# Kernel optimization log

Measured on AMD Instinct MI355X. Metric: run time of the kernel, lower is better.

Reference implementation:

```python
import jax, jax.numpy as jnp
import numpy as np

B, T, D = 4, 2048, 2048
H, G, HD = 16, 4, 128
NB, BS = 512, 16  # num_blocks, block_size
GS = H // G
SCALE = HD ** -0.5
NEG = -1e30


def setup_inputs() -> dict:
    key = jax.random.key(0)
    ks = jax.random.split(key, 5)
    x = jax.random.normal(ks[0], (B, T, D), dtype=jnp.float32)
    block_tables = jnp.arange(B * (T // BS), dtype=jnp.int32).reshape(B, T // BS)
    kv_lens = jnp.zeros((B,), dtype=jnp.int32)
    k_blocks = jnp.zeros((NB, G, BS, HD), jnp.float32)
    v_blocks = jnp.zeros((NB, G, BS, HD), jnp.float32)
    w_q = jax.random.normal(ks[1], (D, H * HD), jnp.float32) * 0.02
    w_k = jax.random.normal(ks[2], (D, G * HD), jnp.float32) * 0.02
    w_v = jax.random.normal(ks[3], (D, G * HD), jnp.float32) * 0.02
    w_o = jax.random.normal(ks[4], (H * HD, D), jnp.float32) * 0.02
    return {"x": x, "w_q": w_q, "w_k": w_k, "w_v": w_v, "w_o": w_o,
            "k_blocks": k_blocks, "v_blocks": v_blocks,
            "block_tables": block_tables, "kv_lens": kv_lens}


def reference(x, w_q, w_k, w_v, w_o, k_blocks, v_blocks, block_tables, kv_lens):
    # projections
    q = (x @ w_q).reshape(B, T, H, HD).transpose(0, 2, 1, 3)   # [B,H,T,Hd]
    k = (x @ w_k).reshape(B, T, G, HD).transpose(0, 2, 1, 3)   # [B,G,T,Hd]
    v = (x @ w_v).reshape(B, T, G, HD).transpose(0, 2, 1, 3)

    # paged cache append (vectorized scatter over [B,T])
    pos = kv_lens[:, None] + jnp.arange(T)                     # [B,T]
    slot, off = pos // BS, pos % BS
    bid = jnp.take_along_axis(block_tables, slot, axis=1)      # [B,T] block ids
    k_blocks = k_blocks.at[bid, :, off, :].set(k.transpose(0, 2, 1, 3))
    v_blocks = v_blocks.at[bid, :, off, :].set(v.transpose(0, 2, 1, 3))

    # gather contiguous KV per request; prefill: kv_lens == 0 -> seq_len = T
    S = T
    nb = (S + BS - 1) // BS
    blk = block_tables[:, :nb]                                 # [B,nb]
    k_seq = k_blocks[blk].transpose(0, 2, 1, 3, 4).reshape(B, G, nb * BS, HD)[:, :, :S]
    v_seq = v_blocks[blk].transpose(0, 2, 1, 3, 4).reshape(B, G, nb * BS, HD)[:, :, :S]

    # original's flat reshapes pair head h with kv group (h % G)
    qg = q.reshape(B, GS, G, T, HD)
    scores = jnp.einsum('bjgqd,bgkd->bjgqk', qg, k_seq) * SCALE

    q_pos = (S - T) + jnp.arange(T)
    k_pos = jnp.arange(S)
    causal = k_pos[None, :] <= q_pos[:, None]                  # [T,S]
    scores = jnp.where(causal, scores, NEG)
    attn = jax.nn.softmax(scores, axis=-1)

    out = jnp.einsum('bjgqk,bgkd->bjgqd', attn, v_seq)         # [B,GS,G,T,Hd]
    out = out.reshape(B, H, T, HD).transpose(0, 2, 1, 3).reshape(B, T, H * HD)
    return out @ w_o
```

## Files before the change

### kernel.cpp

```cpp
#include <hip/hip_runtime.h>
#include <stdint.h>

typedef __attribute__((ext_vector_type(8))) short short8;
typedef __attribute__((ext_vector_type(8))) unsigned short ushort8;
typedef __attribute__((ext_vector_type(4))) float f32x4;

__device__ __forceinline__ ushort f2bf(float f) {
  union { float f; uint32_t u; } v; v.f = f;
  uint32_t r = v.u + 0x7FFFu + ((v.u >> 16) & 1u);
  return (ushort)(r >> 16);
}

__device__ __forceinline__ ushort f2bf_trunc(float f) {
  union { float f; uint32_t u; } v; v.f = f;
  return (ushort)(v.u >> 16);
}

__device__ __forceinline__ float fexp2(float x) {
  float r;
  asm("v_exp_f32 %0, %1" : "=v"(r) : "v"(x));
  return r;
}

__device__ __forceinline__ void gld16(const ushort* g, ushort* l) {
  __builtin_amdgcn_global_load_lds((const __attribute__((address_space(1))) void*)g,
                                   (__attribute__((address_space(3))) void*)l, 16, 0, 0);
}

__global__ __launch_bounds__(256) void k_f32_to_bf16(const float* __restrict__ in,
                                                     ushort* __restrict__ out, long n) {
  long i = ((long)blockIdx.x * 256 + threadIdx.x) * 8;
  if (i >= n) return;
  float4 a = *(const float4*)(in + i);
  float4 b = *(const float4*)(in + i + 4);
  ushort8 o;
  o[0] = f2bf(a.x); o[1] = f2bf(a.y); o[2] = f2bf(a.z); o[3] = f2bf(a.w);
  o[4] = f2bf(b.x); o[5] = f2bf(b.y); o[6] = f2bf(b.z); o[7] = f2bf(b.w);
  *(ushort8*)(out + i) = o;
}

__global__ __launch_bounds__(256) void k_w_transpose(const float* __restrict__ in,
                                                     ushort* __restrict__ out, int R, int C) {
  __shared__ float t[32][33];
  int tx = threadIdx.x & 31, ty = threadIdx.x >> 5;
  int r0 = blockIdx.y * 32, c0 = blockIdx.x * 32;
#pragma unroll
  for (int i = 0; i < 4; i++)
    t[ty + i * 8][tx] = in[(size_t)(r0 + ty + i * 8) * C + c0 + tx];
  __syncthreads();
#pragma unroll
  for (int i = 0; i < 4; i++)
    out[(size_t)(c0 + ty + i * 8) * R + r0 + tx] = f2bf(t[tx][ty + i * 8]);
}

__global__ __launch_bounds__(256) void k_v_transpose(const ushort* __restrict__ qkv,
                                                     ushort* __restrict__ out) {
  __shared__ ushort t[32][33];
  int tx = threadIdx.x & 31, ty = threadIdx.x >> 5;
  int t0 = blockIdx.x * 32, d0 = blockIdx.y * 32;
  int b = blockIdx.z >> 2, g = blockIdx.z & 3;
#pragma unroll
  for (int i = 0; i < 4; i++)
    t[ty + i * 8][tx] =
        qkv[((size_t)b * 2048 + t0 + ty + i * 8) * 3072 + 2560 + g * 128 + d0 + tx];
  __syncthreads();
#pragma unroll
  for (int i = 0; i < 4; i++)
    out[(((size_t)b * 4 + g) * 128 + d0 + ty + i * 8) * 2048 + t0 + tx] = t[tx][ty + i * 8];
}

__device__ __forceinline__ void stage256(const ushort* G, int ldg, ushort* Ls, int tid) {
  int l = tid & 63, w = tid >> 6;
  int rsub = l >> 3;
  int cs = ((l & 7) ^ rsub) << 3;
#pragma unroll
  for (int n = 0; n < 4; n++) {
    int c = n * 8 + w;
    gld16(G + (size_t)(c * 8 + rsub) * ldg + cs, Ls + c * 512 + l * 8);
  }
}

template <int F32OUT>
__global__ __launch_bounds__(512) void k_gemm256(const ushort* __restrict__ A,
                                                 const ushort* __restrict__ BT,
                                                 void* __restrict__ C, int M, int N, int K) {
  __shared__ ushort As0[256 * 64], As1[256 * 64];
  __shared__ ushort Bs0[256 * 64], Bs1[256 * 64];
  const int tid = threadIdx.x;
  const int lane = tid & 63, wid = tid >> 6;
  const int wm = wid >> 2, wn = wid & 3;
  const int l15 = lane & 15, l4 = lane >> 4;
  const int rsw = (l15 & 7) << 3;
  int nwg = gridDim.x * gridDim.y;
  int lin = blockIdx.y * gridDim.x + blockIdx.x;
  int swz = (lin & 7) * (nwg >> 3) + (lin >> 3);
  int bx = swz % gridDim.x, by = swz / gridDim.x;
  const int m0 = by * 256, n0 = bx * 256;

  const ushort* Atile = A + (size_t)m0 * K;
  const ushort* Btile = BT + (size_t)n0 * K;
  const int NK = K >> 6;

  f32x4 acc[8][4] = {};

  stage256(Atile, K, As0, tid);
  stage256(Btile, K, Bs0, tid);
  stage256(Atile + 64, K, As1, tid);
  stage256(Btile + 64, K, Bs1, tid);
  asm volatile("s_waitcnt vmcnt(8)" ::: "memory");
  asm volatile("s_barrier" ::: "memory");

  for (int kt = 0; kt < NK; ++kt) {
    const ushort* Ab = (kt & 1) ? As1 : As0;
    const ushort* Bb = (kt & 1) ? Bs1 : Bs0;
    short8 bfrag[4][2];
#pragma unroll
    for (int nf = 0; nf < 4; nf++)
#pragma unroll
      for (int ks = 0; ks < 2; ks++)
        bfrag[nf][ks] = *(const short8*)&Bb[(wn * 64 + nf * 16 + l15) * 64 +
                                            ((ks * 32 + l4 * 8) ^ rsw)];
#pragma unroll
    for (int q = 0; q < 4; q++) {
      short8 afr[2][2];
#pragma unroll
      for (int dm = 0; dm < 2; dm++)
#pragma unroll
        for (int ks = 0; ks < 2; ks++)
          afr[dm][ks] = *(const short8*)&Ab[(wm * 128 + (q * 2 + dm) * 16 + l15) * 64 +
                                            ((ks * 32 + l4 * 8) ^ rsw)];
      __builtin_amdgcn_s_setprio(1);
#pragma unroll
      for (int dm = 0; dm < 2; dm++)
#pragma unroll
        for (int nf = 0; nf < 4; nf++)
#pragma unroll
          for (int ks = 0; ks < 2; ks++)
            acc[q * 2 + dm][nf] = __builtin_amdgcn_mfma_f32_16x16x32_bf16(
                afr[dm][ks], bfrag[nf][ks], acc[q * 2 + dm][nf], 0, 0, 0);
      __builtin_amdgcn_s_setprio(0);
    }
    asm volatile("s_barrier" ::: "memory");
    if (kt + 2 < NK) {
      stage256(Atile + (kt + 2) * 64, K, (kt & 1) ? As1 : As0, tid);
      stage256(Btile + (kt + 2) * 64, K, (kt & 1) ? Bs1 : Bs0, tid);
      asm volatile("s_waitcnt vmcnt(8)" ::: "memory");
    } else {
      asm volatile("s_waitcnt vmcnt(0)" ::: "memory");
    }
    asm volatile("s_barrier" ::: "memory");
  }

#pragma unroll
  for (int mf = 0; mf < 8; mf++)
#pragma unroll
    for (int nf = 0; nf < 4; nf++)
#pragma unroll
      for (int r = 0; r < 4; r++) {
        int m = m0 + wm * 128 + mf * 16 + l4 * 4 + r;
        int n = n0 + wn * 64 + nf * 16 + l15;
        if (F32OUT)
          ((float*)C)[(size_t)m * N + n] = acc[mf][nf][r];
        else
          ((ushort*)C)[(size_t)m * N + n] = f2bf(acc[mf][nf][r]);
      }
}

__device__ __forceinline__ void stage_k8(const ushort* Kt, ushort* Ks, int tid) {
  int l = tid & 63, w = tid >> 6;
#pragma unroll
  for (int n = 0; n < 2; n++) {
    int cidx = w * 2 + n;
    int r = cidx * 4 + (l >> 4);
    int cs = ((l & 15) * 8) ^ ((r & 7) << 3);
    gld16(Kt + (size_t)r * 3072 + cs, Ks + cidx * 512 + l * 8);
  }
}

__device__ __forceinline__ void stage_v8(const ushort* Vt, ushort* Vs, int tid) {
  int l = tid & 63, w = tid >> 6;
#pragma unroll
  for (int n = 0; n < 2; n++) {
    int cidx = w * 2 + n;
    int d = cidx * 8 + (l >> 3);
    int cs = ((l & 7) * 8) ^ ((d & 7) << 3);
    gld16(Vt + (size_t)d * 2048 + cs, Vs + cidx * 512 + l * 8);
  }
}

__global__ __launch_bounds__(512) void k_attn(const ushort* __restrict__ QKV,
                                              const ushort* __restrict__ VT,
                                              ushort* __restrict__ O) {
  const int T = 2048, HD = 128, G = 4, H = 16, RS = 3072;
  const float SCALE2 = 0.08838834764831845f * 1.4426950408889634f;
  int bid = blockIdx.x;
  int pr = bid >> 6;
  int bh = bid & 63;
  int h = bh & 15, b = bh >> 4;
  int g = h & 3;
  int tid = threadIdx.x, wid = tid >> 6, lane = tid & 63;
  int l15 = lane & 15, l4 = lane >> 4;
  int kswz = (l15 & 7) << 3;

  __shared__ __align__(16) char smem[102400];
  ushort* Ks0 = (ushort*)smem;
  ushort* Ks1 = (ushort*)(smem + 16384);
  ushort* Vs0 = (ushort*)(smem + 32768);
  ushort* Vs1 = (ushort*)(smem + 49152);
  ushort* Pw  = (ushort*)(smem + 65536) + wid * (32 * 72);

  const ushort* Qb = &QKV[(size_t)b * T * RS + h * HD];
  const ushort* Kb = &QKV[(size_t)b * T * RS + 2048 + g * HD];
  const ushort* Vb = &VT[((size_t)b * G + g) * (size_t)HD * T];

#pragma unroll 1
  for (int half = 0; half < 2; half++) {
    int ch = half ? pr : (7 - pr);
    int qw = ch * 256 + wid * 32;
    int nt = 4 * (ch + 1);

    short8 qf[2][4];
#pragma unroll
    for (int mf = 0; mf < 2; mf++)
#pragma unroll
      for (int kf = 0; kf < 4; kf++)
        qf[mf][kf] = *(const short8*)&Qb[(size_t)(qw + mf * 16 + l15) * RS + kf * 32 + l4 * 8];

    f32x4 o[2][8] = {};
    float mrow[8], lrow[8];
#pragma unroll
    for (int i = 0; i < 8; i++) { mrow[i] = -3e38f; lrow[i] = 0.f; }

    stage_k8(Kb, Ks0, tid);
    stage_v8(Vb, Vs0, tid);
    __syncthreads();

#pragma unroll 1
    for (int it = 0; it < nt; ++it) {
      int t0 = it * 64;
      int cur = it & 1;
      ushort* Kc = cur ? Ks1 : Ks0;
      ushort* Vc = cur ? Vs1 : Vs0;
      if (it + 1 < nt) {
        stage_k8(Kb + (size_t)(t0 + 64) * RS, cur ? Ks0 : Ks1, tid);
        stage_v8(Vb + t0 + 64, cur ? Vs0 : Vs1, tid);
      }
      if (t0 <= qw + 31) {
        f32x4 s[2][4] = {};
#pragma unroll
        for (int kf = 0; kf < 4; kf++) {
#pragma unroll
          for (int nf = 0; nf < 4; nf++) {
            short8 bk = *(const short8*)&Kc[(nf * 16 + l15) * 128 + ((kf * 32 + l4 * 8) ^ kswz)];
            s[0][nf] = __builtin_amdgcn_mfma_f32_16x16x32_bf16(qf[0][kf], bk, s[0][nf], 0, 0, 0);
            s[1][nf] = __builtin_amdgcn_mfma_f32_16x16x32_bf16(qf[1][kf], bk, s[1][nf], 0, 0, 0);
          }
        }
        bool needmask = (t0 + 63 > qw);
        if (needmask) {
#pragma unroll
          for (int mf = 0; mf < 2; mf++)
#pragma unroll
            for (int nf = 0; nf < 4; nf++)
#pragma unroll
              for (int r = 0; r < 4; r++) {
                int qq = qw + mf * 16 + l4 * 4 + r;
                int kk = t0 + nf * 16 + l15;
                if (kk > qq) s[mf][nf][r] = -1e30f;
              }
        }
        float xs8[8];
        bool ok = true;
#pragma unroll
        for (int mf = 0; mf < 2; mf++)
#pragma unroll
          for (int r = 0; r < 4; r++) {
            int i = mf * 4 + r;
            float x = fmaxf(fmaxf(s[mf][0][r], s[mf][1][r]), fmaxf(s[mf][2][r], s[mf][3][r]));
            x = fmaxf(x, __shfl_xor(x, 1));
            x = fmaxf(x, __shfl_xor(x, 2));
            x = fmaxf(x, __shfl_xor(x, 4));
            x = fmaxf(x, __shfl_xor(x, 8));
            float xs = x * SCALE2;
            xs8[i] = xs;
            ok = ok && (xs <= mrow[i] + 11.5f);
          }
        if (!__all(ok)) {
#pragma unroll
          for (int i = 0; i < 8; i++) {
            float mn = fmaxf(mrow[i], xs8[i]);
            float sc = fexp2(mrow[i] - mn);
            mrow[i] = mn;
            lrow[i] *= sc;
#pragma unroll
            for (int nfo = 0; nfo < 8; nfo++)
              o[i >> 2][nfo][i & 3] *= sc;
          }
        }
        float rs[8];
#pragma unroll
        for (int i = 0; i < 8; i++) rs[i] = 0.f;
#pragma unroll
        for (int mf = 0; mf < 2; mf++)
#pragma unroll
          for (int nf = 0; nf < 4; nf++)
#pragma unroll
            for (int r = 0; r < 4; r++) {
              float pq = fexp2(__builtin_fmaf(s[mf][nf][r], SCALE2, -mrow[mf * 4 + r]));
              rs[mf * 4 + r] += pq;
              Pw[(mf * 16 + l4 * 4 + r) * 72 + nf * 16 + l15] = f2bf_trunc(pq);
            }
#pragma unroll
        for (int i = 0; i < 8; i++) lrow[i] += rs[i];
#pragma unroll
        for (int kf = 0; kf < 2; kf++) {
          short8 pa0 = *(const short8*)&Pw[(l15) * 72 + kf * 32 + l4 * 8];
          short8 pa1 = *(const short8*)&Pw[(16 + l15) * 72 + kf * 32 + l4 * 8];
#pragma unroll
          for (int nfo = 0; nfo < 8; nfo++) {
            short8 bv = *(const short8*)&Vc[(nfo * 16 + l15) * 64 + ((kf * 32 + l4 * 8) ^ kswz)];
            o[0][nfo] = __builtin_amdgcn_mfma_f32_16x16x32_bf16(pa0, bv, o[0][nfo], 0, 0, 0);
            o[1][nfo] = __builtin_amdgcn_mfma_f32_16x16x32_bf16(pa1, bv, o[1][nfo], 0, 0, 0);
          }
        }
      }
      __syncthreads();
    }

#pragma unroll
    for (int i = 0; i < 8; i++) {
      float x = lrow[i];
      x += __shfl_xor(x, 1);
      x += __shfl_xor(x, 2);
      x += __shfl_xor(x, 4);
      x += __shfl_xor(x, 8);
      lrow[i] = x;
    }
    float inv[8];
#pragma unroll
    for (int i = 0; i < 8; i++) inv[i] = 1.0f / lrow[i];
#pragma unroll
    for (int mf = 0; mf < 2; mf++)
#pragma unroll
      for (int nfo = 0; nfo < 8; nfo++)
#pragma unroll
        for (int r = 0; r < 4; r++) {
          int t = qw + mf * 16 + l4 * 4 + r;
          int d = nfo * 16 + l15;
          O[(((size_t)b * T + t) * H + h) * HD + d] = f2bf(o[mf][nfo][r] * inv[mf * 4 + r]);
        }
    __syncthreads();
  }
}

extern "C" void kernel_launch(void* const* d_in, const int* in_sizes, int n_in,
                              void* d_out, int out_size, void* d_ws, size_t ws_size,
                              hipStream_t stream) {
  const float* x   = (const float*)d_in[0];
  const float* w_q = (const float*)d_in[1];
  const float* w_k = (const float*)d_in[2];
  const float* w_v = (const float*)d_in[3];
  const float* w_o = (const float*)d_in[4];

  char* ws = (char*)d_ws;
  ushort* xbf  = (ushort*)(ws);
  ushort* wkvT = (ushort*)(ws + 33554432ul);
  ushort* woT  = (ushort*)(ws + 46137344ul);
  ushort* qkvb = (ushort*)(ws + 54525952ul);
  ushort* VTb  = (ushort*)(ws + 104857600ul);
  ushort* attn = xbf;

  k_f32_to_bf16<<<8192, 256, 0, stream>>>(x, xbf, 16777216L);
  k_w_transpose<<<dim3(64, 64), 256, 0, stream>>>(w_q, wkvT, 2048, 2048);
  k_w_transpose<<<dim3(16, 64), 256, 0, stream>>>(w_k, wkvT + 2048ul * 2048, 2048, 512);
  k_w_transpose<<<dim3(16, 64), 256, 0, stream>>>(w_v, wkvT + 2560ul * 2048, 2048, 512);
  k_w_transpose<<<dim3(64, 64), 256, 0, stream>>>(w_o, woT, 2048, 2048);

  k_gemm256<0><<<dim3(12, 32), 512, 0, stream>>>(xbf, wkvT, qkvb, 8192, 3072, 2048);

  k_v_transpose<<<dim3(64, 4, 16), 256, 0, stream>>>(qkvb, VTb);

  k_attn<<<256, 512, 0, stream>>>(qkvb, VTb, attn);

  k_gemm256<1><<<dim3(8, 32), 512, 0, stream>>>(attn, woT, (float*)d_out, 8192, 2048, 2048);
}
```

Measured before the change: 358.8 us.

## Restructure GEMM into 4-stage K=32 pipeline with interleaved prefetch

Replaces the double-buffered K=64 GEMM with a four-slot ring of K=32 tiles, prefetching three tiles ahead. Loads are split so the B and A prefetches are issued between the two MFMA halves of each step. The LDS layout changes to a fragment-native ordering with no XOR swizzle, and the vmcnt waits are tuned for the tail. It aims to hide global-load latency better and cut barrier stalls, at the cost of more loop iterations, more barriers per unit of K, and possible LDS bank conflicts from the unswizzled layout.

```diff
diff --git a/kernel.cpp b/kernel.cpp
--- a/kernel.cpp
+++ b/kernel.cpp
@@ -69,85 +69,81 @@
     out[(((size_t)b * 4 + g) * 128 + d0 + ty + i * 8) * 2048 + t0 + tx] = t[tx][ty + i * 8];
 }
 
-__device__ __forceinline__ void stage256(const ushort* G, int ldg, ushort* Ls, int tid) {
-  int l = tid & 63, w = tid >> 6;
-  int rsub = l >> 3;
-  int cs = ((l & 7) ^ rsub) << 3;
-#pragma unroll
-  for (int n = 0; n < 4; n++) {
-    int c = n * 8 + w;
-    gld16(G + (size_t)(c * 8 + rsub) * ldg + cs, Ls + c * 512 + l * 8);
-  }
-}
-
 template <int F32OUT>
-__global__ __launch_bounds__(512) void k_gemm256(const ushort* __restrict__ A,
-                                                 const ushort* __restrict__ BT,
-                                                 void* __restrict__ C, int M, int N, int K) {
-  __shared__ ushort As0[256 * 64], As1[256 * 64];
-  __shared__ ushort Bs0[256 * 64], Bs1[256 * 64];
+__global__ __launch_bounds__(512) void k_gemm256p(const ushort* __restrict__ A,
+                                                  const ushort* __restrict__ BT,
+                                                  void* __restrict__ C, int M, int N, int K) {
+  __shared__ ushort As[4][8192];
+  __shared__ ushort Bs[4][8192];
   const int tid = threadIdx.x;
   const int lane = tid & 63, wid = tid >> 6;
   const int wm = wid >> 2, wn = wid & 3;
   const int l15 = lane & 15, l4 = lane >> 4;
-  const int rsw = (l15 & 7) << 3;
   int nwg = gridDim.x * gridDim.y;
   int lin = blockIdx.y * gridDim.x + blockIdx.x;
   int swz = (lin & 7) * (nwg >> 3) + (lin >> 3);
   int bx = swz % gridDim.x, by = swz / gridDim.x;
   const int m0 = by * 256, n0 = bx * 256;
-
   const ushort* Atile = A + (size_t)m0 * K;
   const ushort* Btile = BT + (size_t)n0 * K;
-  const int NK = K >> 6;
+  const int NK = K >> 5;
 
   f32x4 acc[8][4] = {};
 
-  stage256(Atile, K, As0, tid);
-  stage256(Btile, K, Bs0, tid);
-  stage256(Atile + 64, K, As1, tid);
-  stage256(Btile + 64, K, Bs1, tid);
+  auto stage = [&](const ushort* G, ushort* slot, int t) {
+#pragma unroll
+    for (int n = 0; n < 2; n++) {
+      int c = wid * 2 + n;
+      gld16(G + (size_t)(c * 16 + l15) * K + t * 32 + l4 * 8, slot + c * 512 + lane * 8);
+    }
+  };
+
+  stage(Btile, Bs[0], 0); stage(Atile, As[0], 0);
+  stage(Btile, Bs[1], 1); stage(Atile, As[1], 1);
+  stage(Btile, Bs[2], 2); stage(Atile, As[2], 2);
   asm volatile("s_waitcnt vmcnt(8)" ::: "memory");
   asm volatile("s_barrier" ::: "memory");
 
-  for (int kt = 0; kt < NK; ++kt) {
-    const ushort* Ab = (kt & 1) ? As1 : As0;
-    const ushort* Bb = (kt & 1) ? Bs1 : Bs0;
-    short8 bfrag[4][2];
+#pragma unroll 1
+  for (int t = 0; t < NK; ++t) {
+    const ushort* Ab = As[t & 3];
+    const ushort* Bb = Bs[t & 3];
+    short8 bf[4], af[4];
 #pragma unroll
     for (int nf = 0; nf < 4; nf++)
-#pragma unroll
-      for (int ks = 0; ks < 2; ks++)
-        bfrag[nf][ks] = *(const short8*)&Bb[(wn * 64 + nf * 16 + l15) * 64 +
-                                            ((ks * 32 + l4 * 8) ^ rsw)];
-#pragma unroll
-    for (int q = 0; q < 4; q++) {
-      short8 afr[2][2];
-#pragma unroll
-      for (int dm = 0; dm < 2; dm++)
-#pragma unroll
-        for (int ks = 0; ks < 2; ks++)
-          afr[dm][ks] = *(const short8*)&Ab[(wm * 128 + (q * 2 + dm) * 16 + l15) * 64 +
-                                            ((ks * 32 + l4 * 8) ^ rsw)];
-      __builtin_amdgcn_s_setprio(1);
-#pragma unroll
-      for (int dm = 0; dm < 2; dm++)
-#pragma unroll
-        for (int nf = 0; nf < 4; nf++)
-#pragma unroll
-          for (int ks = 0; ks < 2; ks++)
-            acc[q * 2 + dm][nf] = __builtin_amdgcn_mfma_f32_16x16x32_bf16(
-                afr[dm][ks], bfrag[nf][ks], acc[q * 2 + dm][nf], 0, 0, 0);
-      __builtin_amdgcn_s_setprio(0);
-    }
-    asm volatile("s_barrier" ::: "memory");
-    if (kt + 2 < NK) {
-      stage256(Atile + (kt + 2) * 64, K, (kt & 1) ? As1 : As0, tid);
-      stage256(Btile + (kt + 2) * 64, K, (kt & 1) ? Bs1 : Bs0, tid);
-      asm volatile("s_waitcnt vmcnt(8)" ::: "memory");
-    } else {
-      asm volatile("s_waitcnt vmcnt(0)" ::: "memory");
-    }
+      bf[nf] = *(const short8*)&Bb[(wn * 4 + nf) * 512 + l4 * 128 + l15 * 8];
+#pragma unroll
+    for (int mf = 0; mf < 4; mf++)
+      af[mf] = *(const short8*)&Ab[(wm * 8 + mf) * 512 + l4 * 128 + l15 * 8];
+    asm volatile("s_waitcnt lgkmcnt(0)" ::: "memory");
+    __builtin_amdgcn_sched_barrier(0);
+    if (t + 3 < NK) stage(Btile, Bs[(t + 3) & 3], t + 3);
+    __builtin_amdgcn_s_setprio(1);
+#pragma unroll
+    for (int mf = 0; mf < 4; mf++)
+#pragma unroll
+      for (int nf = 0; nf < 4; nf++)
+        acc[mf][nf] =
+            __builtin_amdgcn_mfma_f32_16x16x32_bf16(af[mf], bf[nf], acc[mf][nf], 0, 0, 0);
+    __builtin_amdgcn_s_setprio(0);
+#pragma unroll
+    for (int mf = 0; mf < 4; mf++)
+      af[mf] = *(const short8*)&Ab[(wm * 8 + 4 + mf) * 512 + l4 * 128 + l15 * 8];
+    asm volatile("s_waitcnt lgkmcnt(0)" ::: "memory");
+    __builtin_amdgcn_sched_barrier(0);
+    if (t + 3 < NK) stage(Atile, As[(t + 3) & 3], t + 3);
+    __builtin_amdgcn_s_setprio(1);
+#pragma unroll
+    for (int mf = 0; mf < 4; mf++)
+#pragma unroll
+      for (int nf = 0; nf < 4; nf++)
+        acc[4 + mf][nf] =
+            __builtin_amdgcn_mfma_f32_16x16x32_bf16(af[mf], bf[nf], acc[4 + mf][nf], 0, 0, 0);
+    __builtin_amdgcn_s_setprio(0);
+    int fl = NK - 2 - t;
+    if (fl >= 2)      { asm volatile("s_waitcnt vmcnt(8)" ::: "memory"); }
+    else if (fl == 1) { asm volatile("s_waitcnt vmcnt(4)" ::: "memory"); }
+    else if (fl == 0) { asm volatile("s_waitcnt vmcnt(0)" ::: "memory"); }
     asm volatile("s_barrier" ::: "memory");
   }
 
@@ -376,11 +372,11 @@
   k_w_transpose<<<dim3(16, 64), 256, 0, stream>>>(w_v, wkvT + 2560ul * 2048, 2048, 512);
   k_w_transpose<<<dim3(64, 64), 256, 0, stream>>>(w_o, woT, 2048, 2048);
 
-  k_gemm256<0><<<dim3(12, 32), 512, 0, stream>>>(xbf, wkvT, qkvb, 8192, 3072, 2048);
+  k_gemm256p<0><<<dim3(12, 32), 512, 0, stream>>>(xbf, wkvT, qkvb, 8192, 3072, 2048);
 
   k_v_transpose<<<dim3(64, 4, 16), 256, 0, stream>>>(qkvb, VTb);
 
   k_attn<<<256, 512, 0, stream>>>(qkvb, VTb, attn);
 
-  k_gemm256<1><<<dim3(8, 32), 512, 0, stream>>>(attn, woT, (float*)d_out, 8192, 2048, 2048);
-}
+  k_gemm256p<1><<<dim3(8, 32), 512, 0, stream>>>(attn, woT, (float*)d_out, 8192, 2048, 2048);
+}
```

Result: slower. 374.8 us (+4.5%).
